# Optimization experiments

Measured on AMD Instinct MI355X. Metric: run time of the kernel, lower is better.

The kernel has to match this reference:

```python
import jax, jax.numpy as jnp
import numpy as np
import math

INPUT_SIZE = 1024
B, L1, L2 = 8, 2048, 2048


def setup_inputs() -> dict:
    key = jax.random.key(0)
    ks = jax.random.split(key, 10)
    s = 1.0 / math.sqrt(INPUT_SIZE)
    return {
        "Q": jax.random.normal(ks[0], (B, L1, INPUT_SIZE), dtype=jnp.float32),
        "K": jax.random.normal(ks[1], (B, L2, INPUT_SIZE), dtype=jnp.float32),
        "V": jax.random.normal(ks[2], (B, L2, INPUT_SIZE), dtype=jnp.float32),
        "K_mask": jax.random.randint(ks[3], (B, L2), 0, 2, dtype=jnp.int32),
        "Wq": jax.random.normal(ks[4], (INPUT_SIZE, INPUT_SIZE), dtype=jnp.float32) * s,
        "bq": jax.random.normal(ks[5], (INPUT_SIZE,), dtype=jnp.float32) * s,
        "Wk": jax.random.normal(ks[6], (INPUT_SIZE, INPUT_SIZE), dtype=jnp.float32) * s,
        "bk": jax.random.normal(ks[7], (INPUT_SIZE,), dtype=jnp.float32) * s,
        "Wv": jax.random.normal(ks[8], (INPUT_SIZE, INPUT_SIZE), dtype=jnp.float32) * s,
        "bv": jax.random.normal(ks[9], (INPUT_SIZE,), dtype=jnp.float32) * s,
    }


def reference(Q, K, V, K_mask, Wq, bq, Wk, bk, Wv, bv):
    # Linear projections (torch Linear: x @ W.T + b)
    q = jnp.einsum('bld,ed->ble', Q, Wq) + bq
    k = jnp.einsum('bld,ed->ble', K, Wk) + bk
    v = jnp.einsum('bld,ed->ble', V, Wv) + bv
    # scores: [B, L1, L2], scaled by sqrt(input_size)
    scores = jnp.einsum('bqd,bkd->bqk', q, k) / math.sqrt(INPUT_SIZE)
    # K_mask == 1 marks padding -> -inf before softmax
    scores = jnp.where(K_mask[:, None, :] == 1, -jnp.inf, scores)
    alpha = jax.nn.softmax(scores, axis=-1)
    matched_seq = jnp.einsum('bqk,bkd->bqd', alpha, v)
    return matched_seq
```

## Files before the change

kernel.cpp:

```cpp
#include <hip/hip_runtime.h>


using u16 = unsigned short;
using frag_ab = __attribute__((ext_vector_type(8))) short;
using frag_cd = __attribute__((ext_vector_type(4))) float;

#define BAR() asm volatile("s_barrier" ::: "memory")
#define WAITV(n) asm volatile("s_waitcnt vmcnt(" #n ")" ::: "memory")
#define L(d, ab, h) (lds + (((d) * 4) + ((ab) * 2) + (h)) * 8192)

__device__ __forceinline__ u16 f2bf(float f) {
  union { float f; unsigned u; } c; c.f = f;
  unsigned u = c.u;
  return (u16)((u + 0x7FFFu + ((u >> 16) & 1u)) >> 16);
}

__device__ __forceinline__ void async_ld16(const void* g, void* l) {
  __builtin_amdgcn_global_load_lds(
      (const __attribute__((address_space(1))) unsigned*)g,
      (__attribute__((address_space(3))) unsigned*)l, 16, 0, 0);
}

__global__ void cvt_f32_bf16(const float* __restrict__ in, u16* __restrict__ out, long n) {
  long i = ((long)blockIdx.x * 256 + threadIdx.x) * 4;
  if (i >= n) return;
  float4 v = *reinterpret_cast<const float4*>(in + i);
  ushort4 o = make_ushort4(f2bf(v.x), f2bf(v.y), f2bf(v.z), f2bf(v.w));
  *reinterpret_cast<ushort4*>(out + i) = o;
}

__device__ __forceinline__ void stage_half(const u16* __restrict__ g_rowbase,
                                           long Kstr, u16* l_half,
                                           int wave, int lane) {
  const int t = wave * 64 + lane;
  #pragma unroll
  for (int i = 0; i < 2; i++) {
    const int row = i * 64 + (t >> 3);
    const int cb  = (t & 7) * 16;
    const int cbs = cb ^ ((row & 7) << 4);
    async_ld16(g_rowbase + (long)row * Kstr + (cbs >> 1),
               l_half + i * 4096 + wave * 512);
  }
}

__device__ __forceinline__ frag_ab ld_frag(const u16* half_base, int r, int k) {
  const int idx = r * 64 + (k ^ ((r & 7) << 3));
  return *reinterpret_cast<const frag_ab*>(half_base + idx);
}

template<int OUT_MODE>
__device__ __forceinline__ void
gemm256_body(const u16* __restrict__ A, const u16* __restrict__ Bt,
             void* __restrict__ Cout, const float* __restrict__ bias,
             int M, int N, int K, long sA, long sB, long sC, float scale,
             u16* lds)
{
  const int gx = gridDim.x, gy = gridDim.y, gz = gridDim.z;
  const int nwg = gx * gy * gz;
  const int lin = ((int)blockIdx.z * gy + blockIdx.y) * gx + blockIdx.x;
  const int q8 = nwg >> 3, r8 = nwg & 7;
  const int xcd = lin & 7, idx8 = lin >> 3;
  const int swz = (xcd < r8 ? xcd * (q8 + 1) : r8 * (q8 + 1) + (xcd - r8) * q8) + idx8;
  const int z = swz / (gx * gy);
  const int rem = swz % (gx * gy);
  const int m0 = (rem / gx) * 256;
  const int n0 = (rem % gx) * 256;

  const u16* Ab = A + (long)z * sA;
  const u16* Bb = Bt + (long)z * sB;

  const int tid = threadIdx.x;
  const int wave = tid >> 6, lane = tid & 63;
  const int wm = wave >> 2;
  const int wn = wave & 3;
  const int ln15 = lane & 15, kof = (lane >> 4) * 8;
  const int rB0 = (wn & 1) * 64;
  const int NT = K >> 6;

  frag_cd acc[8][4];
  #pragma unroll
  for (int i = 0; i < 8; i++)
    #pragma unroll
    for (int j = 0; j < 4; j++)
      acc[i][j] = (frag_cd){0.f, 0.f, 0.f, 0.f};

  stage_half(Ab + (long)(m0 +   0) * K, K, L(0, 0, 0), wave, lane);
  stage_half(Ab + (long)(m0 + 128) * K, K, L(0, 0, 1), wave, lane);
  stage_half(Bb + (long)(n0 +   0) * K, K, L(0, 1, 0), wave, lane);
  stage_half(Bb + (long)(n0 + 128) * K, K, L(0, 1, 1), wave, lane);
  {
    const int t1 = (1 < NT) ? 1 : 0;
    stage_half(Bb + (long)(n0 +   0) * K + t1 * 64, K, L(1, 1, 0), wave, lane);
    stage_half(Bb + (long)(n0 + 128) * K + t1 * 64, K, L(1, 1, 1), wave, lane);
  }
  WAITV(4);
  BAR();

  for (int t = 0; t < NT; ++t) {
    const int d = t & 1;
    const u16* Al = L(d, 0, wm);
    const u16* Bl = L(d, 1, wn >> 1);
    const int tA = (t + 1 < NT) ? t + 1 : NT - 1;
    const int tB = (t + 2 < NT) ? t + 2 : NT - 1;

    frag_ab bf[4][2], af[2][2];

    #pragma unroll
    for (int bn = 0; bn < 4; ++bn)
      #pragma unroll
      for (int kk = 0; kk < 2; ++kk)
        bf[bn][kk] = ld_frag(Bl, rB0 + bn * 16 + ln15, kk * 32 + kof);
    #pragma unroll
    for (int am = 0; am < 2; ++am)
      #pragma unroll
      for (int kk = 0; kk < 2; ++kk)
        af[am][kk] = ld_frag(Al, am * 16 + ln15, kk * 32 + kof);
    stage_half(Ab + (long)(m0 +   0) * K + tA * 64, K, L(d ^ 1, 0, 0), wave, lane);
    stage_half(Ab + (long)(m0 + 128) * K + tA * 64, K, L(d ^ 1, 0, 1), wave, lane);
    BAR();
    __builtin_amdgcn_s_setprio(1);
    #pragma unroll
    for (int am = 0; am < 2; ++am)
      #pragma unroll
      for (int bn = 0; bn < 4; ++bn)
        #pragma unroll
        for (int kk = 0; kk < 2; ++kk)
          acc[am][bn] = __builtin_amdgcn_mfma_f32_16x16x32_bf16(af[am][kk], bf[bn][kk], acc[am][bn], 0, 0, 0);
    __builtin_amdgcn_s_setprio(0);
    BAR();

    #pragma unroll
    for (int am = 0; am < 2; ++am)
      #pragma unroll
      for (int kk = 0; kk < 2; ++kk)
        af[am][kk] = ld_frag(Al, (2 + am) * 16 + ln15, kk * 32 + kof);
    stage_half(Bb + (long)(n0 + 0) * K + tB * 64, K, L(d, 1, 0), wave, lane);
    BAR();
    __builtin_amdgcn_s_setprio(1);
    #pragma unroll
    for (int am = 0; am < 2; ++am)
      #pragma unroll
      for (int bn = 0; bn < 4; ++bn)
        #pragma unroll
        for (int kk = 0; kk < 2; ++kk)
          acc[2 + am][bn] = __builtin_amdgcn_mfma_f32_16x16x32_bf16(af[am][kk], bf[bn][kk], acc[2 + am][bn], 0, 0, 0);
    __builtin_amdgcn_s_setprio(0);
    BAR();

    #pragma unroll
    for (int am = 0; am < 2; ++am)
      #pragma unroll
      for (int kk = 0; kk < 2; ++kk)
        af[am][kk] = ld_frag(Al, (4 + am) * 16 + ln15, kk * 32 + kof);
    stage_half(Bb + (long)(n0 + 128) * K + tB * 64, K, L(d, 1, 1), wave, lane);
    BAR();
    __builtin_amdgcn_s_setprio(1);
    #pragma unroll
    for (int am = 0; am < 2; ++am)
      #pragma unroll
      for (int bn = 0; bn < 4; ++bn)
        #pragma unroll
        for (int kk = 0; kk < 2; ++kk)
          acc[4 + am][bn] = __builtin_amdgcn_mfma_f32_16x16x32_bf16(af[am][kk], bf[bn][kk], acc[4 + am][bn], 0, 0, 0);
    __builtin_amdgcn_s_setprio(0);
    BAR();

    #pragma unroll
    for (int am = 0; am < 2; ++am)
      #pragma unroll
      for (int kk = 0; kk < 2; ++kk)
        af[am][kk] = ld_frag(Al, (6 + am) * 16 + ln15, kk * 32 + kof);
    BAR();
    __builtin_amdgcn_s_setprio(1);
    #pragma unroll
    for (int am = 0; am < 2; ++am)
      #pragma unroll
      for (int bn = 0; bn < 4; ++bn)
        #pragma unroll
        for (int kk = 0; kk < 2; ++kk)
          acc[6 + am][bn] = __builtin_amdgcn_mfma_f32_16x16x32_bf16(af[am][kk], bf[bn][kk], acc[6 + am][bn], 0, 0, 0);
    __builtin_amdgcn_s_setprio(0);
    WAITV(4);
    BAR();
  }

  WAITV(0);
  BAR();

  const int cl = lane & 15;
  const int rb = (lane >> 4) * 4;
  #pragma unroll
  for (int bn = 0; bn < 4; ++bn) {
    const int gcol = n0 + wn * 64 + bn * 16 + cl;
    const float badd = bias ? bias[gcol] : 0.f;
    #pragma unroll
    for (int am = 0; am < 8; ++am) {
      #pragma unroll
      for (int r = 0; r < 4; ++r) {
        const int grow = m0 + wm * 128 + am * 16 + rb + r;
        const float val = acc[am][bn][r] * scale + badd;
        if (OUT_MODE == 0) {
          ((float*)Cout)[(long)z * sC + (long)grow * N + gcol] = val;
        } else if (OUT_MODE == 1) {
          ((u16*)Cout)[(long)z * sC + (long)grow * N + gcol] = f2bf(val);
        } else {
          const int bb = grow >> 11, l2 = grow & 2047;
          ((u16*)Cout)[((long)bb * N + gcol) * 2048 + l2] = f2bf(val);
        }
      }
    }
  }
}

__global__ void __launch_bounds__(512, 2)
proj_gemm(const u16* A, const u16* Bt, void* C, const float* bias,
          int M, int N, int K, long sA, long sB, long sC, float scale) {
  __shared__ u16 lds[8 * 8192];
  gemm256_body<1>(A, Bt, C, bias, M, N, K, sA, sB, sC, scale, lds);
}
__global__ void __launch_bounds__(512, 2)
projv_gemm(const u16* A, const u16* Bt, void* C, const float* bias,
           int M, int N, int K, long sA, long sB, long sC, float scale) {
  __shared__ u16 lds[8 * 8192];
  gemm256_body<2>(A, Bt, C, bias, M, N, K, sA, sB, sC, scale, lds);
}
__global__ void __launch_bounds__(512, 2)
qk_gemm(const u16* A, const u16* Bt, void* C, const float* bias,
        int M, int N, int K, long sA, long sB, long sC, float scale) {
  __shared__ u16 lds[8 * 8192];
  gemm256_body<0>(A, Bt, C, bias, M, N, K, sA, sB, sC, scale, lds);
}
__global__ void __launch_bounds__(512, 2)
pv_gemm(const u16* A, const u16* Bt, void* C, const float* bias,
        int M, int N, int K, long sA, long sB, long sC, float scale) {
  __shared__ u16 lds[8 * 8192];
  gemm256_body<0>(A, Bt, C, bias, M, N, K, sA, sB, sC, scale, lds);
}

__global__ void softmax_rows(const float* __restrict__ S, const int* __restrict__ Km,
                             u16* __restrict__ P)
{
  const long row = blockIdx.x;
  const int b = (int)(row >> 11);
  const float* s = S + row * 2048;
  const int* mask = Km + (long)b * 2048;
  u16* p = P + row * 2048;

  const int t = threadIdx.x;
  const int base = t * 8;

  float4 v0 = *reinterpret_cast<const float4*>(s + base);
  float4 v1 = *reinterpret_cast<const float4*>(s + base + 4);
  int4 mA = *reinterpret_cast<const int4*>(mask + base);
  int4 mB = *reinterpret_cast<const int4*>(mask + base + 4);

  float vals[8] = {v0.x, v0.y, v0.z, v0.w, v1.x, v1.y, v1.z, v1.w};
  const int mk[8] = {mA.x, mA.y, mA.z, mA.w, mB.x, mB.y, mB.z, mB.w};

  float mx = -3.0e38f;
  #pragma unroll
  for (int i = 0; i < 8; i++) if (!mk[i]) mx = fmaxf(mx, vals[i]);
  #pragma unroll
  for (int off = 32; off > 0; off >>= 1) mx = fmaxf(mx, __shfl_xor(mx, off));

  __shared__ float redm[4], reds[4];
  const int wave = t >> 6, lane = t & 63;
  if (lane == 0) redm[wave] = mx;
  __syncthreads();
  mx = fmaxf(fmaxf(redm[0], redm[1]), fmaxf(redm[2], redm[3]));

  float e[8]; float sum = 0.f;
  #pragma unroll
  for (int i = 0; i < 8; i++) { e[i] = mk[i] ? 0.f : __expf(vals[i] - mx); sum += e[i]; }
  #pragma unroll
  for (int off = 32; off > 0; off >>= 1) sum += __shfl_xor(sum, off);
  if (lane == 0) reds[wave] = sum;
  __syncthreads();
  sum = reds[0] + reds[1] + reds[2] + reds[3];
  const float inv = 1.f / sum;

  ushort4 o0 = make_ushort4(f2bf(e[0]*inv), f2bf(e[1]*inv), f2bf(e[2]*inv), f2bf(e[3]*inv));
  ushort4 o1 = make_ushort4(f2bf(e[4]*inv), f2bf(e[5]*inv), f2bf(e[6]*inv), f2bf(e[7]*inv));
  *reinterpret_cast<ushort4*>(p + base) = o0;
  *reinterpret_cast<ushort4*>(p + base + 4) = o1;
}

extern "C" void kernel_launch(void* const* d_in, const int* in_sizes, int n_in,
                              void* d_out, int out_size, void* d_ws, size_t ws_size,
                              hipStream_t stream) {
  (void)in_sizes; (void)n_in; (void)out_size;

  const float* Qin  = (const float*)d_in[0];
  const float* Kin  = (const float*)d_in[1];
  const float* Vin  = (const float*)d_in[2];
  const int*   Kmask = (const int*)d_in[3];
  const float* Wq = (const float*)d_in[4];
  const float* bq = (const float*)d_in[5];
  const float* Wk = (const float*)d_in[6];
  const float* bk = (const float*)d_in[7];
  const float* Wv = (const float*)d_in[8];
  const float* bv = (const float*)d_in[9];

  char* ws = (char*)d_ws;
  const size_t MB = 1024UL * 1024UL;
  const long NQKV = 8L * 2048 * 1024;
  const long NW = 1024L * 1024;
  const dim3 blk(256);
  const dim3 gblk(512);
  const float rs = 0.03125f;

  if (ws_size >= 226 * MB) {
    u16*  qb = (u16*)(ws);
    u16*  kb = (u16*)(ws + 32 * MB);
    u16*  vT = (u16*)(ws + 64 * MB);
    u16*  P  = (u16*)(ws + 96 * MB);
    u16*  Xb = (u16*)(ws + 96 * MB);
    float* S = (float*)(ws + 160 * MB);
    u16*  Wb = (u16*)(ws + 224 * MB);

    cvt_f32_bf16<<<dim3(NQKV / 1024), blk, 0, stream>>>(Qin, Xb, NQKV);
    cvt_f32_bf16<<<dim3(NW / 1024), blk, 0, stream>>>(Wq, Wb, NW);
    proj_gemm<<<dim3(4, 64, 1), gblk, 0, stream>>>(Xb, Wb, qb, bq,
        16384, 1024, 1024, 0, 0, 0, 1.f);

    cvt_f32_bf16<<<dim3(NQKV / 1024), blk, 0, stream>>>(Kin, Xb, NQKV);
    cvt_f32_bf16<<<dim3(NW / 1024), blk, 0, stream>>>(Wk, Wb, NW);
    proj_gemm<<<dim3(4, 64, 1), gblk, 0, stream>>>(Xb, Wb, kb, bk,
        16384, 1024, 1024, 0, 0, 0, 1.f);

    cvt_f32_bf16<<<dim3(NQKV / 1024), blk, 0, stream>>>(Vin, Xb, NQKV);
    cvt_f32_bf16<<<dim3(NW / 1024), blk, 0, stream>>>(Wv, Wb, NW);
    projv_gemm<<<dim3(4, 64, 1), gblk, 0, stream>>>(Xb, Wb, vT, bv,
        16384, 1024, 1024, 0, 0, 0, 1.f);

    for (int h = 0; h < 2; h++) {
      const u16* qbH = qb + (long)(4 * h) * 2048 * 1024;
      const u16* kbH = kb + (long)(4 * h) * 2048 * 1024;
      qk_gemm<<<dim3(8, 8, 4), gblk, 0, stream>>>(qbH, kbH, S, nullptr,
          2048, 2048, 1024, 2048L * 1024, 2048L * 1024, 2048L * 2048, rs);
      softmax_rows<<<dim3(8192), blk, 0, stream>>>(
          S, Kmask + (long)(4 * h) * 2048, P + (long)(4 * h) * 2048 * 2048);
    }

    pv_gemm<<<dim3(4, 8, 8), gblk, 0, stream>>>(P, vT, d_out, nullptr,
        2048, 1024, 2048, 2048L * 2048, 1024L * 2048, 2048L * 1024, 1.f);
  } else if (ws_size >= 194 * MB) {
    u16*  qb = (u16*)(ws);
    u16*  kb = (u16*)(ws + 32 * MB);
    u16*  vT = (u16*)(ws + 64 * MB);
    u16*  P  = (u16*)(ws + 96 * MB);
    u16*  Xb = (u16*)(ws + 96 * MB);
    float* S = (float*)(ws + 160 * MB);
    u16*  Wb = (u16*)(ws + 192 * MB);

    cvt_f32_bf16<<<dim3(NQKV / 1024), blk, 0, stream>>>(Qin, Xb, NQKV);
    cvt_f32_bf16<<<dim3(NW / 1024), blk, 0, stream>>>(Wq, Wb, NW);
    proj_gemm<<<dim3(4, 64, 1), gblk, 0, stream>>>(Xb, Wb, qb, bq,
        16384, 1024, 1024, 0, 0, 0, 1.f);

    cvt_f32_bf16<<<dim3(NQKV / 1024), blk, 0, stream>>>(Kin, Xb, NQKV);
    cvt_f32_bf16<<<dim3(NW / 1024), blk, 0, stream>>>(Wk, Wb, NW);
    proj_gemm<<<dim3(4, 64, 1), gblk, 0, stream>>>(Xb, Wb, kb, bk,
        16384, 1024, 1024, 0, 0, 0, 1.f);

    cvt_f32_bf16<<<dim3(NQKV / 1024), blk, 0, stream>>>(Vin, Xb, NQKV);
    cvt_f32_bf16<<<dim3(NW / 1024), blk, 0, stream>>>(Wv, Wb, NW);
    projv_gemm<<<dim3(4, 64, 1), gblk, 0, stream>>>(Xb, Wb, vT, bv,
        16384, 1024, 1024, 0, 0, 0, 1.f);

    for (int p = 0; p < 4; p++) {
      const u16* qbP = qb + (long)(2 * p) * 2048 * 1024;
      const u16* kbP = kb + (long)(2 * p) * 2048 * 1024;
      qk_gemm<<<dim3(8, 8, 2), gblk, 0, stream>>>(qbP, kbP, S, nullptr,
          2048, 2048, 1024, 2048L * 1024, 2048L * 1024, 2048L * 2048, rs);
      softmax_rows<<<dim3(4096), blk, 0, stream>>>(
          S, Kmask + (long)(2 * p) * 2048, P + (long)(2 * p) * 2048 * 2048);
    }

    pv_gemm<<<dim3(4, 8, 8), gblk, 0, stream>>>(P, vT, d_out, nullptr,
        2048, 1024, 2048, 2048L * 2048, 1024L * 2048, 2048L * 1024, 1.f);
  } else {
    u16*  qb = (u16*)(ws);
    u16*  kb = (u16*)(ws + 32 * MB);
    u16*  vT = (u16*)(ws + 64 * MB);
    u16*  Xb = (u16*)(ws + 96 * MB);
    float* S = (float*)(ws + 96 * MB);
    u16*  P  = (u16*)(ws + 112 * MB);
    u16*  Wb = (u16*)(ws + 128 * MB);

    cvt_f32_bf16<<<dim3(NQKV / 1024), blk, 0, stream>>>(Qin, Xb, NQKV);
    cvt_f32_bf16<<<dim3(NW / 1024), blk, 0, stream>>>(Wq, Wb, NW);
    proj_gemm<<<dim3(4, 64, 1), gblk, 0, stream>>>(Xb, Wb, qb, bq,
        16384, 1024, 1024, 0, 0, 0, 1.f);

    cvt_f32_bf16<<<dim3(NQKV / 1024), blk, 0, stream>>>(Kin, Xb, NQKV);
    cvt_f32_bf16<<<dim3(NW / 1024), blk, 0, stream>>>(Wk, Wb, NW);
    proj_gemm<<<dim3(4, 64, 1), gblk, 0, stream>>>(Xb, Wb, kb, bk,
        16384, 1024, 1024, 0, 0, 0, 1.f);

    cvt_f32_bf16<<<dim3(NQKV / 1024), blk, 0, stream>>>(Vin, Xb, NQKV);
    cvt_f32_bf16<<<dim3(NW / 1024), blk, 0, stream>>>(Wv, Wb, NW);
    projv_gemm<<<dim3(4, 64, 1), gblk, 0, stream>>>(Xb, Wb, vT, bv,
        16384, 1024, 1024, 0, 0, 0, 1.f);

    for (int b = 0; b < 8; b++) {
      const u16* qbB = qb + (long)b * 2048 * 1024;
      const u16* kbB = kb + (long)b * 2048 * 1024;
      const u16* vTB = vT + (long)b * 1024 * 2048;
      float* outB = (float*)d_out + (long)b * 2048 * 1024;

      qk_gemm<<<dim3(8, 8, 1), gblk, 0, stream>>>(qbB, kbB, S, nullptr,
          2048, 2048, 1024, 0, 0, 0, rs);
      softmax_rows<<<dim3(2048), blk, 0, stream>>>(S, Kmask + (long)b * 2048, P);
      pv_gemm<<<dim3(4, 8, 1), gblk, 0, stream>>>(P, vTB, outB, nullptr,
          2048, 1024, 2048, 0, 0, 0, 1.f);
    }
  }
}
```

Measured before the change: 383.1 us.

## Fuse fp32-to-bf16 activation conversion into projection GEMM A-tile loads

The projection GEMMs now read fp32 Q/K/V directly. Each thread loads float4 pairs into registers, packs them to bf16 and writes them into the swizzled LDS tile, interleaved with the MFMA phases. This removes three separate conversion kernels and their round trips through the 32MB bf16 staging buffer. In exchange the projection kernels drop to one workgroup per CU through launch bounds, use more registers, and lose the async direct-to-LDS path for A.

Result: slower. 405.1 us (+5.8%).

```diff
diff --git a/kernel.cpp b/kernel.cpp
--- a/kernel.cpp
+++ b/kernel.cpp
@@ -7,12 +7,23 @@
 
 #define BAR() asm volatile("s_barrier" ::: "memory")
 #define WAITV(n) asm volatile("s_waitcnt vmcnt(" #n ")" ::: "memory")
+#define WAITLGKM0() do { asm volatile("s_waitcnt lgkmcnt(0)" ::: "memory"); \
+                         __builtin_amdgcn_sched_barrier(0); } while (0)
 #define L(d, ab, h) (lds + (((d) * 4) + ((ab) * 2) + (h)) * 8192)
 
 __device__ __forceinline__ u16 f2bf(float f) {
   union { float f; unsigned u; } c; c.f = f;
   unsigned u = c.u;
   return (u16)((u + 0x7FFFu + ((u >> 16) & 1u)) >> 16);
+}
+
+__device__ __forceinline__ frag_ab pack8(float4 x, float4 y) {
+  frag_ab p;
+  p[0] = (short)f2bf(x.x); p[1] = (short)f2bf(x.y);
+  p[2] = (short)f2bf(x.z); p[3] = (short)f2bf(x.w);
+  p[4] = (short)f2bf(y.x); p[5] = (short)f2bf(y.y);
+  p[6] = (short)f2bf(y.z); p[7] = (short)f2bf(y.w);
+  return p;
 }
 
 __device__ __forceinline__ void async_ld16(const void* g, void* l) {
@@ -48,9 +59,13 @@
   return *reinterpret_cast<const frag_ab*>(half_base + idx);
 }
 
-template<int OUT_MODE>
+__device__ __forceinline__ void st_frag(u16* half_base, int r, int s, frag_ab v) {
+  *reinterpret_cast<frag_ab*>(half_base + r * 64 + ((s ^ (r & 7)) << 3)) = v;
+}
+
+template<int OUT_MODE, bool AF32>
 __device__ __forceinline__ void
-gemm256_body(const u16* __restrict__ A, const u16* __restrict__ Bt,
+gemm256_body(const void* __restrict__ Avoid, const u16* __restrict__ Bt,
              void* __restrict__ Cout, const float* __restrict__ bias,
              int M, int N, int K, long sA, long sB, long sC, float scale,
              u16* lds)
@@ -66,7 +81,8 @@
   const int m0 = (rem / gx) * 256;
   const int n0 = (rem % gx) * 256;
 
-  const u16* Ab = A + (long)z * sA;
+  const u16*   Ab16 = AF32 ? nullptr : (const u16*)Avoid + (long)z * sA;
+  const float* Abf  = AF32 ? (const float*)Avoid + (long)z * sA : nullptr;
   const u16* Bb = Bt + (long)z * sB;
 
   const int tid = threadIdx.x;
@@ -76,6 +92,8 @@
   const int ln15 = lane & 15, kof = (lane >> 4) * 8;
   const int rB0 = (wn & 1) * 64;
   const int NT = K >> 6;
+  const int sr = tid >> 3;
+  const int ss = tid & 7;
 
   frag_cd acc[8][4];
   #pragma unroll
@@ -84,17 +102,43 @@
     for (int j = 0; j < 4; j++)
       acc[i][j] = (frag_cd){0.f, 0.f, 0.f, 0.f};
 
-  stage_half(Ab + (long)(m0 +   0) * K, K, L(0, 0, 0), wave, lane);
-  stage_half(Ab + (long)(m0 + 128) * K, K, L(0, 0, 1), wave, lane);
-  stage_half(Bb + (long)(n0 +   0) * K, K, L(0, 1, 0), wave, lane);
-  stage_half(Bb + (long)(n0 + 128) * K, K, L(0, 1, 1), wave, lane);
-  {
-    const int t1 = (1 < NT) ? 1 : 0;
-    stage_half(Bb + (long)(n0 +   0) * K + t1 * 64, K, L(1, 1, 0), wave, lane);
-    stage_half(Bb + (long)(n0 + 128) * K + t1 * 64, K, L(1, 1, 1), wave, lane);
+  if (AF32) {
+    const float* a0 = Abf + (long)(m0 + sr) * K + ss * 8;
+    float4 c0a = *(const float4*)(a0);
+    float4 c0b = *(const float4*)(a0 + 4);
+    float4 c1a = *(const float4*)(a0 +  64L * K);
+    float4 c1b = *(const float4*)(a0 +  64L * K + 4);
+    float4 c2a = *(const float4*)(a0 + 128L * K);
+    float4 c2b = *(const float4*)(a0 + 128L * K + 4);
+    float4 c3a = *(const float4*)(a0 + 192L * K);
+    float4 c3b = *(const float4*)(a0 + 192L * K + 4);
+    stage_half(Bb + (long)(n0 +   0) * K, K, L(0, 1, 0), wave, lane);
+    stage_half(Bb + (long)(n0 + 128) * K, K, L(0, 1, 1), wave, lane);
+    {
+      const int t1 = (1 < NT) ? 1 : 0;
+      stage_half(Bb + (long)(n0 +   0) * K + t1 * 64, K, L(1, 1, 0), wave, lane);
+      stage_half(Bb + (long)(n0 + 128) * K + t1 * 64, K, L(1, 1, 1), wave, lane);
+    }
+    st_frag(L(0, 0, 0), sr,      ss, pack8(c0a, c0b));
+    st_frag(L(0, 0, 0), sr + 64, ss, pack8(c1a, c1b));
+    st_frag(L(0, 0, 1), sr,      ss, pack8(c2a, c2b));
+    st_frag(L(0, 0, 1), sr + 64, ss, pack8(c3a, c3b));
+    WAITV(0);
+    WAITLGKM0();
+    BAR();
+  } else {
+    stage_half(Ab16 + (long)(m0 +   0) * K, K, L(0, 0, 0), wave, lane);
+    stage_half(Ab16 + (long)(m0 + 128) * K, K, L(0, 0, 1), wave, lane);
+    stage_half(Bb + (long)(n0 +   0) * K, K, L(0, 1, 0), wave, lane);
+    stage_half(Bb + (long)(n0 + 128) * K, K, L(0, 1, 1), wave, lane);
+    {
+      const int t1 = (1 < NT) ? 1 : 0;
+      stage_half(Bb + (long)(n0 +   0) * K + t1 * 64, K, L(1, 1, 0), wave, lane);
+      stage_half(Bb + (long)(n0 + 128) * K + t1 * 64, K, L(1, 1, 1), wave, lane);
+    }
+    WAITV(4);
+    BAR();
   }
-  WAITV(4);
-  BAR();
 
   for (int t = 0; t < NT; ++t) {
     const int d = t & 1;
@@ -104,6 +148,7 @@
     const int tB = (t + 2 < NT) ? t + 2 : NT - 1;
 
     frag_ab bf[4][2], af[2][2];
+    float4 c0a, c0b, c1a, c1b, c2a, c2b, c3a, c3b;
 
     #pragma unroll
     for (int bn = 0; bn < 4; ++bn)
@@ -115,8 +160,16 @@
       #pragma unroll
       for (int kk = 0; kk < 2; ++kk)
         af[am][kk] = ld_frag(Al, am * 16 + ln15, kk * 32 + kof);
-    stage_half(Ab + (long)(m0 +   0) * K + tA * 64, K, L(d ^ 1, 0, 0), wave, lane);
-    stage_half(Ab + (long)(m0 + 128) * K + tA * 64, K, L(d ^ 1, 0, 1), wave, lane);
+    if (AF32) {
+      const float* ap = Abf + (long)(m0 + sr) * K + tA * 64 + ss * 8;
+      c0a = *(const float4*)(ap);
+      c0b = *(const float4*)(ap + 4);
+      c1a = *(const float4*)(ap + 64L * K);
+      c1b = *(const float4*)(ap + 64L * K + 4);
+    } else {
+      stage_half(Ab16 + (long)(m0 +   0) * K + tA * 64, K, L(d ^ 1, 0, 0), wave, lane);
+      stage_half(Ab16 + (long)(m0 + 128) * K + tA * 64, K, L(d ^ 1, 0, 1), wave, lane);
+    }
     BAR();
     __builtin_amdgcn_s_setprio(1);
     #pragma unroll
@@ -134,7 +187,18 @@
       #pragma unroll
       for (int kk = 0; kk < 2; ++kk)
         af[am][kk] = ld_frag(Al, (2 + am) * 16 + ln15, kk * 32 + kof);
+    if (AF32) {
+      const float* ap = Abf + (long)(m0 + 128 + sr) * K + tA * 64 + ss * 8;
+      c2a = *(const float4*)(ap);
+      c2b = *(const float4*)(ap + 4);
+      c3a = *(const float4*)(ap + 64L * K);
+      c3b = *(const float4*)(ap + 64L * K + 4);
+    }
     stage_half(Bb + (long)(n0 + 0) * K + tB * 64, K, L(d, 1, 0), wave, lane);
+    if (AF32) {
+      st_frag(L(d ^ 1, 0, 0), sr,      ss, pack8(c0a, c0b));
+      st_frag(L(d ^ 1, 0, 0), sr + 64, ss, pack8(c1a, c1b));
+    }
     BAR();
     __builtin_amdgcn_s_setprio(1);
     #pragma unroll
@@ -153,6 +217,11 @@
       for (int kk = 0; kk < 2; ++kk)
         af[am][kk] = ld_frag(Al, (4 + am) * 16 + ln15, kk * 32 + kof);
     stage_half(Bb + (long)(n0 + 128) * K + tB * 64, K, L(d, 1, 1), wave, lane);
+    if (AF32) {
+      st_frag(L(d ^ 1, 0, 1), sr,      ss, pack8(c2a, c2b));
+      st_frag(L(d ^ 1, 0, 1), sr + 64, ss, pack8(c3a, c3b));
+      WAITLGKM0();
+    }
     BAR();
     __builtin_amdgcn_s_setprio(1);
     #pragma unroll
@@ -180,7 +249,7 @@
         for (int kk = 0; kk < 2; ++kk)
           acc[6 + am][bn] = __builtin_amdgcn_mfma_f32_16x16x32_bf16(af[am][kk], bf[bn][kk], acc[6 + am][bn], 0, 0, 0);
     __builtin_amdgcn_s_setprio(0);
-    WAITV(4);
+    if (!AF32) { WAITV(4); }
     BAR();
   }
 
@@ -212,29 +281,29 @@
   }
 }
 
-__global__ void __launch_bounds__(512, 2)
-proj_gemm(const u16* A, const u16* Bt, void* C, const float* bias,
+__global__ void __launch_bounds__(512, 1)
+proj_gemm(const void* A, const u16* Bt, void* C, const float* bias,
           int M, int N, int K, long sA, long sB, long sC, float scale) {
   __shared__ u16 lds[8 * 8192];
-  gemm256_body<1>(A, Bt, C, bias, M, N, K, sA, sB, sC, scale, lds);
-}
-__global__ void __launch_bounds__(512, 2)
-projv_gemm(const u16* A, const u16* Bt, void* C, const float* bias,
+  gemm256_body<1, true>(A, Bt, C, bias, M, N, K, sA, sB, sC, scale, lds);
+}
+__global__ void __launch_bounds__(512, 1)
+projv_gemm(const void* A, const u16* Bt, void* C, const float* bias,
            int M, int N, int K, long sA, long sB, long sC, float scale) {
   __shared__ u16 lds[8 * 8192];
-  gemm256_body<2>(A, Bt, C, bias, M, N, K, sA, sB, sC, scale, lds);
+  gemm256_body<2, true>(A, Bt, C, bias, M, N, K, sA, sB, sC, scale, lds);
 }
 __global__ void __launch_bounds__(512, 2)
-qk_gemm(const u16* A, const u16* Bt, void* C, const float* bias,
+qk_gemm(const void* A, const u16* Bt, void* C, const float* bias,
         int M, int N, int K, long sA, long sB, long sC, float scale) {
   __shared__ u16 lds[8 * 8192];
-  gemm256_body<0>(A, Bt, C, bias, M, N, K, sA, sB, sC, scale, lds);
+  gemm256_body<0, false>(A, Bt, C, bias, M, N, K, sA, sB, sC, scale, lds);
 }
 __global__ void __launch_bounds__(512, 2)
-pv_gemm(const u16* A, const u16* Bt, void* C, const float* bias,
+pv_gemm(const void* A, const u16* Bt, void* C, const float* bias,
         int M, int N, int K, long sA, long sB, long sC, float scale) {
   __shared__ u16 lds[8 * 8192];
-  gemm256_body<0>(A, Bt, C, bias, M, N, K, sA, sB, sC, scale, lds);
+  gemm256_body<0, false>(A, Bt, C, bias, M, N, K, sA, sB, sC, scale, lds);
 }
 
 __global__ void softmax_rows(const float* __restrict__ S, const int* __restrict__ Km,
@@ -303,7 +372,6 @@
 
   char* ws = (char*)d_ws;
   const size_t MB = 1024UL * 1024UL;
-  const long NQKV = 8L * 2048 * 1024;
   const long NW = 1024L * 1024;
   const dim3 blk(256);
   const dim3 gblk(512);
@@ -314,23 +382,19 @@
     u16*  kb = (u16*)(ws + 32 * MB);
     u16*  vT = (u16*)(ws + 64 * MB);
     u16*  P  = (u16*)(ws + 96 * MB);
-    u16*  Xb = (u16*)(ws + 96 * MB);
     float* S = (float*)(ws + 160 * MB);
     u16*  Wb = (u16*)(ws + 224 * MB);
 
-    cvt_f32_bf16<<<dim3(NQKV / 1024), blk, 0, stream>>>(Qin, Xb, NQKV);
     cvt_f32_bf16<<<dim3(NW / 1024), blk, 0, stream>>>(Wq, Wb, NW);
-    proj_gemm<<<dim3(4, 64, 1), gblk, 0, stream>>>(Xb, Wb, qb, bq,
-        16384, 1024, 1024, 0, 0, 0, 1.f);
-
-    cvt_f32_bf16<<<dim3(NQKV / 1024), blk, 0, stream>>>(Kin, Xb, NQKV);
+    proj_gemm<<<dim3(4, 64, 1), gblk, 0, stream>>>(Qin, Wb, qb, bq,
+        16384, 1024, 1024, 0, 0, 0, 1.f);
+
     cvt_f32_bf16<<<dim3(NW / 1024), blk, 0, stream>>>(Wk, Wb, NW);
-    proj_gemm<<<dim3(4, 64, 1), gblk, 0, stream>>>(Xb, Wb, kb, bk,
-        16384, 1024, 1024, 0, 0, 0, 1.f);
-
-    cvt_f32_bf16<<<dim3(NQKV / 1024), blk, 0, stream>>>(Vin, Xb, NQKV);
+    proj_gemm<<<dim3(4, 64, 1), gblk, 0, stream>>>(Kin, Wb, kb, bk,
+        16384, 1024, 1024, 0, 0, 0, 1.f);
+
     cvt_f32_bf16<<<dim3(NW / 1024), blk, 0, stream>>>(Wv, Wb, NW);
-    projv_gemm<<<dim3(4, 64, 1), gblk, 0, stream>>>(Xb, Wb, vT, bv,
+    projv_gemm<<<dim3(4, 64, 1), gblk, 0, stream>>>(Vin, Wb, vT, bv,
         16384, 1024, 1024, 0, 0, 0, 1.f);
 
     for (int h = 0; h < 2; h++) {
@@ -349,23 +413,17 @@
     u16*  kb = (u16*)(ws + 32 * MB);
     u16*  vT = (u16*)(ws + 64 * MB);
     u16*  P  = (u16*)(ws + 96 * MB);
-    u16*  Xb = (u16*)(ws + 96 * MB);
     float* S = (float*)(ws + 160 * MB);
     u16*  Wb = (u16*)(ws + 192 * MB);
 
-    cvt_f32_bf16<<<dim3(NQKV / 1024), blk, 0, stream>>>(Qin, Xb, NQKV);
     cvt_f32_bf16<<<dim3(NW / 1024), blk, 0, stream>>>(Wq, Wb, NW);
-    proj_gemm<<<dim3(4, 64, 1), gblk, 0, stream>>>(Xb, Wb, qb, bq,
-        16384, 1024, 1024, 0, 0, 0, 1.f);
-
-    cvt_f32_bf16<<<dim3(NQKV / 1024), blk, 0, stream>>>(Kin, Xb, NQKV);
+    proj_gemm<<<dim3(4, 64, 1), gblk, 0, stream>>>(Qin, Wb, qb, bq,
+        16384, 1024, 1024, 0, 0, 0, 1.f);
     cvt_f32_bf16<<<dim3(NW / 1024), blk, 0, stream>>>(Wk, Wb, NW);
-    proj_gemm<<<dim3(4, 64, 1), gblk, 0, stream>>>(Xb, Wb, kb, bk,
-        16384, 1024, 1024, 0, 0, 0, 1.f);
-
-    cvt_f32_bf16<<<dim3(NQKV / 1024), blk, 0, stream>>>(Vin, Xb, NQKV);
+    proj_gemm<<<dim3(4, 64, 1), gblk, 0, stream>>>(Kin, Wb, kb, bk,
+        16384, 1024, 1024, 0, 0, 0, 1.f);
     cvt_f32_bf16<<<dim3(NW / 1024), blk, 0, stream>>>(Wv, Wb, NW);
-    projv_gemm<<<dim3(4, 64, 1), gblk, 0, stream>>>(Xb, Wb, vT, bv,
+    projv_gemm<<<dim3(4, 64, 1), gblk, 0, stream>>>(Vin, Wb, vT, bv,
         16384, 1024, 1024, 0, 0, 0, 1.f);
 
     for (int p = 0; p < 4; p++) {
@@ -383,24 +441,18 @@
     u16*  qb = (u16*)(ws);
     u16*  kb = (u16*)(ws + 32 * MB);
     u16*  vT = (u16*)(ws + 64 * MB);
-    u16*  Xb = (u16*)(ws + 96 * MB);
-    float* S = (float*)(ws + 96 * MB);
-    u16*  P  = (u16*)(ws + 112 * MB);
-    u16*  Wb = (u16*)(ws + 128 * MB);
-
-    cvt_f32_bf16<<<dim3(NQKV / 1024), blk, 0, stream>>>(Qin, Xb, NQKV);
+    float* S = (float*)(ws + 96 * MB + 2 * MB);
+    u16*  P  = (u16*)(ws + 96 * MB + 18 * MB);
+    u16*  Wb = (u16*)(ws + 96 * MB);
+
     cvt_f32_bf16<<<dim3(NW / 1024), blk, 0, stream>>>(Wq, Wb, NW);
-    proj_gemm<<<dim3(4, 64, 1), gblk, 0, stream>>>(Xb, Wb, qb, bq,
-        16384, 1024, 1024, 0, 0, 0, 1.f);
-
-    cvt_f32_bf16<<<dim3(NQKV / 1024), blk, 0, stream>>>(Kin, Xb, NQKV);
+    proj_gemm<<<dim3(4, 64, 1), gblk, 0, stream>>>(Qin, Wb, qb, bq,
+        16384, 1024, 1024, 0, 0, 0, 1.f);
     cvt_f32_bf16<<<dim3(NW / 1024), blk, 0, stream>>>(Wk, Wb, NW);
-    proj_gemm<<<dim3(4, 64, 1), gblk, 0, stream>>>(Xb, Wb, kb, bk,
-        16384, 1024, 1024, 0, 0, 0, 1.f);
-
-    cvt_f32_bf16<<<dim3(NQKV / 1024), blk, 0, stream>>>(Vin, Xb, NQKV);
+    proj_gemm<<<dim3(4, 64, 1), gblk, 0, stream>>>(Kin, Wb, kb, bk,
+        16384, 1024, 1024, 0, 0, 0, 1.f);
     cvt_f32_bf16<<<dim3(NW / 1024), blk, 0, stream>>>(Wv, Wb, NW);
-    projv_gemm<<<dim3(4, 64, 1), gblk, 0, stream>>>(Xb, Wb, vT, bv,
+    projv_gemm<<<dim3(4, 64, 1), gblk, 0, stream>>>(Vin, Wb, vT, bv,
         16384, 1024, 1024, 0, 0, 0, 1.f);
 
     for (int b = 0; b < 8; b++) {
```

## Store attention scores in fp16 and batch input conversion and QK launches

Applied to the files above, without the earlier changes.

The QK GEMM now writes scores as fp16 instead of fp32, and the softmax reads fp16. This halves the bytes of the largest intermediate written and then read back. The three fp32-to-bf16 input conversions are merged into one launch writing separate buffers. With the larger workspace, all 8 batches of the QK GEMM and softmax run in one launch each instead of a loop. The costs are some precision loss in the scores and extra workspace overlap that depends on launch ordering.

New measurement: 365.3 us. 1.05x faster.

```diff
diff --git a/kernel.cpp b/kernel.cpp
--- a/kernel.cpp
+++ b/kernel.cpp
@@ -14,6 +14,12 @@
   unsigned u = c.u;
   return (u16)((u + 0x7FFFu + ((u >> 16) & 1u)) >> 16);
 }
+__device__ __forceinline__ u16 f2h(float f) {
+  union { _Float16 h; u16 u; } c; c.h = (_Float16)f; return c.u;
+}
+__device__ __forceinline__ float h2f(u16 u) {
+  union { u16 u; _Float16 h; } c; c.u = u; return (float)c.h;
+}
 
 __device__ __forceinline__ void async_ld16(const void* g, void* l) {
   __builtin_amdgcn_global_load_lds(
@@ -25,8 +31,18 @@
   long i = ((long)blockIdx.x * 256 + threadIdx.x) * 4;
   if (i >= n) return;
   float4 v = *reinterpret_cast<const float4*>(in + i);
-  ushort4 o = make_ushort4(f2bf(v.x), f2bf(v.y), f2bf(v.z), f2bf(v.w));
-  *reinterpret_cast<ushort4*>(out + i) = o;
+  *reinterpret_cast<ushort4*>(out + i) =
+      make_ushort4(f2bf(v.x), f2bf(v.y), f2bf(v.z), f2bf(v.w));
+}
+
+__global__ void cvt3_f32_bf16(const float* __restrict__ q, const float* __restrict__ k,
+                              const float* __restrict__ v, u16* __restrict__ out) {
+  const float* in = blockIdx.z == 0 ? q : (blockIdx.z == 1 ? k : v);
+  u16* o = out + (long)blockIdx.z * 16777216L;
+  long i = ((long)blockIdx.x * 256 + threadIdx.x) * 4;
+  float4 x = *reinterpret_cast<const float4*>(in + i);
+  *reinterpret_cast<ushort4*>(o + i) =
+      make_ushort4(f2bf(x.x), f2bf(x.y), f2bf(x.z), f2bf(x.w));
 }
 
 __device__ __forceinline__ void stage_half(const u16* __restrict__ g_rowbase,
@@ -203,6 +219,8 @@
           ((float*)Cout)[(long)z * sC + (long)grow * N + gcol] = val;
         } else if (OUT_MODE == 1) {
           ((u16*)Cout)[(long)z * sC + (long)grow * N + gcol] = f2bf(val);
+        } else if (OUT_MODE == 3) {
+          ((u16*)Cout)[(long)z * sC + (long)grow * N + gcol] = f2h(val);
         } else {
           const int bb = grow >> 11, l2 = grow & 2047;
           ((u16*)Cout)[((long)bb * N + gcol) * 2048 + l2] = f2bf(val);
@@ -228,7 +246,7 @@
 qk_gemm(const u16* A, const u16* Bt, void* C, const float* bias,
         int M, int N, int K, long sA, long sB, long sC, float scale) {
   __shared__ u16 lds[8 * 8192];
-  gemm256_body<0>(A, Bt, C, bias, M, N, K, sA, sB, sC, scale, lds);
+  gemm256_body<3>(A, Bt, C, bias, M, N, K, sA, sB, sC, scale, lds);
 }
 __global__ void __launch_bounds__(512, 2)
 pv_gemm(const u16* A, const u16* Bt, void* C, const float* bias,
@@ -237,24 +255,25 @@
   gemm256_body<0>(A, Bt, C, bias, M, N, K, sA, sB, sC, scale, lds);
 }
 
-__global__ void softmax_rows(const float* __restrict__ S, const int* __restrict__ Km,
-                             u16* __restrict__ P)
+__global__ void softmax_rows_h(const u16* __restrict__ S, const int* __restrict__ Km,
+                               u16* __restrict__ P)
 {
   const long row = blockIdx.x;
   const int b = (int)(row >> 11);
-  const float* s = S + row * 2048;
+  const u16* s = S + row * 2048;
   const int* mask = Km + (long)b * 2048;
   u16* p = P + row * 2048;
 
   const int t = threadIdx.x;
   const int base = t * 8;
 
-  float4 v0 = *reinterpret_cast<const float4*>(s + base);
-  float4 v1 = *reinterpret_cast<const float4*>(s + base + 4);
+  ushort4 r0 = *reinterpret_cast<const ushort4*>(s + base);
+  ushort4 r1 = *reinterpret_cast<const ushort4*>(s + base + 4);
   int4 mA = *reinterpret_cast<const int4*>(mask + base);
   int4 mB = *reinterpret_cast<const int4*>(mask + base + 4);
 
-  float vals[8] = {v0.x, v0.y, v0.z, v0.w, v1.x, v1.y, v1.z, v1.w};
+  float vals[8] = {h2f(r0.x), h2f(r0.y), h2f(r0.z), h2f(r0.w),
+                   h2f(r1.x), h2f(r1.y), h2f(r1.z), h2f(r1.w)};
   const int mk[8] = {mA.x, mA.y, mA.z, mA.w, mB.x, mB.y, mB.z, mB.w};
 
   float mx = -3.0e38f;
@@ -279,10 +298,10 @@
   sum = reds[0] + reds[1] + reds[2] + reds[3];
   const float inv = 1.f / sum;
 
-  ushort4 o0 = make_ushort4(f2bf(e[0]*inv), f2bf(e[1]*inv), f2bf(e[2]*inv), f2bf(e[3]*inv));
-  ushort4 o1 = make_ushort4(f2bf(e[4]*inv), f2bf(e[5]*inv), f2bf(e[6]*inv), f2bf(e[7]*inv));
-  *reinterpret_cast<ushort4*>(p + base) = o0;
-  *reinterpret_cast<ushort4*>(p + base + 4) = o1;
+  *reinterpret_cast<ushort4*>(p + base) =
+      make_ushort4(f2bf(e[0]*inv), f2bf(e[1]*inv), f2bf(e[2]*inv), f2bf(e[3]*inv));
+  *reinterpret_cast<ushort4*>(p + base + 4) =
+      make_ushort4(f2bf(e[4]*inv), f2bf(e[5]*inv), f2bf(e[6]*inv), f2bf(e[7]*inv));
 }
 
 extern "C" void kernel_launch(void* const* d_in, const int* in_sizes, int n_in,
@@ -303,7 +322,6 @@
 
   char* ws = (char*)d_ws;
   const size_t MB = 1024UL * 1024UL;
-  const long NQKV = 8L * 2048 * 1024;
   const long NW = 1024L * 1024;
   const dim3 blk(256);
   const dim3 gblk(512);
@@ -314,33 +332,27 @@
     u16*  kb = (u16*)(ws + 32 * MB);
     u16*  vT = (u16*)(ws + 64 * MB);
     u16*  P  = (u16*)(ws + 96 * MB);
-    u16*  Xb = (u16*)(ws + 96 * MB);
-    float* S = (float*)(ws + 160 * MB);
+    u16*  Xq = (u16*)(ws + 96 * MB);
+    u16*  S  = (u16*)(ws + 160 * MB);
     u16*  Wb = (u16*)(ws + 224 * MB);
 
-    cvt_f32_bf16<<<dim3(NQKV / 1024), blk, 0, stream>>>(Qin, Xb, NQKV);
+    cvt3_f32_bf16<<<dim3(16384, 1, 3), blk, 0, stream>>>(Qin, Kin, Vin, Xq);
+
     cvt_f32_bf16<<<dim3(NW / 1024), blk, 0, stream>>>(Wq, Wb, NW);
-    proj_gemm<<<dim3(4, 64, 1), gblk, 0, stream>>>(Xb, Wb, qb, bq,
-        16384, 1024, 1024, 0, 0, 0, 1.f);
-
-    cvt_f32_bf16<<<dim3(NQKV / 1024), blk, 0, stream>>>(Kin, Xb, NQKV);
+    proj_gemm<<<dim3(4, 64, 1), gblk, 0, stream>>>(Xq, Wb, qb, bq,
+        16384, 1024, 1024, 0, 0, 0, 1.f);
+
     cvt_f32_bf16<<<dim3(NW / 1024), blk, 0, stream>>>(Wk, Wb, NW);
-    proj_gemm<<<dim3(4, 64, 1), gblk, 0, stream>>>(Xb, Wb, kb, bk,
-        16384, 1024, 1024, 0, 0, 0, 1.f);
-
-    cvt_f32_bf16<<<dim3(NQKV / 1024), blk, 0, stream>>>(Vin, Xb, NQKV);
+    proj_gemm<<<dim3(4, 64, 1), gblk, 0, stream>>>(Xq + 16777216L, Wb, kb, bk,
+        16384, 1024, 1024, 0, 0, 0, 1.f);
+
     cvt_f32_bf16<<<dim3(NW / 1024), blk, 0, stream>>>(Wv, Wb, NW);
-    projv_gemm<<<dim3(4, 64, 1), gblk, 0, stream>>>(Xb, Wb, vT, bv,
-        16384, 1024, 1024, 0, 0, 0, 1.f);
-
-    for (int h = 0; h < 2; h++) {
-      const u16* qbH = qb + (long)(4 * h) * 2048 * 1024;
-      const u16* kbH = kb + (long)(4 * h) * 2048 * 1024;
-      qk_gemm<<<dim3(8, 8, 4), gblk, 0, stream>>>(qbH, kbH, S, nullptr,
-          2048, 2048, 1024, 2048L * 1024, 2048L * 1024, 2048L * 2048, rs);
-      softmax_rows<<<dim3(8192), blk, 0, stream>>>(
-          S, Kmask + (long)(4 * h) * 2048, P + (long)(4 * h) * 2048 * 2048);
-    }
+    projv_gemm<<<dim3(4, 64, 1), gblk, 0, stream>>>(Xq + 2L * 16777216L, Wb, vT, bv,
+        16384, 1024, 1024, 0, 0, 0, 1.f);
+
+    qk_gemm<<<dim3(8, 8, 8), gblk, 0, stream>>>(qb, kb, S, nullptr,
+        2048, 2048, 1024, 2048L * 1024, 2048L * 1024, 2048L * 2048, rs);
+    softmax_rows_h<<<dim3(16384), blk, 0, stream>>>(S, Kmask, P);
 
     pv_gemm<<<dim3(4, 8, 8), gblk, 0, stream>>>(P, vT, d_out, nullptr,
         2048, 1024, 2048, 2048L * 2048, 1024L * 2048, 2048L * 1024, 1.f);
@@ -349,32 +361,29 @@
     u16*  kb = (u16*)(ws + 32 * MB);
     u16*  vT = (u16*)(ws + 64 * MB);
     u16*  P  = (u16*)(ws + 96 * MB);
-    u16*  Xb = (u16*)(ws + 96 * MB);
-    float* S = (float*)(ws + 160 * MB);
+    u16*  Xq = (u16*)(ws + 96 * MB);
+    u16*  S  = (u16*)(ws + 160 * MB);
     u16*  Wb = (u16*)(ws + 192 * MB);
 
-    cvt_f32_bf16<<<dim3(NQKV / 1024), blk, 0, stream>>>(Qin, Xb, NQKV);
+    cvt3_f32_bf16<<<dim3(16384, 1, 3), blk, 0, stream>>>(Qin, Kin, Vin, Xq);
+
     cvt_f32_bf16<<<dim3(NW / 1024), blk, 0, stream>>>(Wq, Wb, NW);
-    proj_gemm<<<dim3(4, 64, 1), gblk, 0, stream>>>(Xb, Wb, qb, bq,
-        16384, 1024, 1024, 0, 0, 0, 1.f);
-
-    cvt_f32_bf16<<<dim3(NQKV / 1024), blk, 0, stream>>>(Kin, Xb, NQKV);
+    proj_gemm<<<dim3(4, 64, 1), gblk, 0, stream>>>(Xq, Wb, qb, bq,
+        16384, 1024, 1024, 0, 0, 0, 1.f);
     cvt_f32_bf16<<<dim3(NW / 1024), blk, 0, stream>>>(Wk, Wb, NW);
-    proj_gemm<<<dim3(4, 64, 1), gblk, 0, stream>>>(Xb, Wb, kb, bk,
-        16384, 1024, 1024, 0, 0, 0, 1.f);
-
-    cvt_f32_bf16<<<dim3(NQKV / 1024), blk, 0, stream>>>(Vin, Xb, NQKV);
+    proj_gemm<<<dim3(4, 64, 1), gblk, 0, stream>>>(Xq + 16777216L, Wb, kb, bk,
+        16384, 1024, 1024, 0, 0, 0, 1.f);
     cvt_f32_bf16<<<dim3(NW / 1024), blk, 0, stream>>>(Wv, Wb, NW);
-    projv_gemm<<<dim3(4, 64, 1), gblk, 0, stream>>>(Xb, Wb, vT, bv,
-        16384, 1024, 1024, 0, 0, 0, 1.f);
-
-    for (int p = 0; p < 4; p++) {
-      const u16* qbP = qb + (long)(2 * p) * 2048 * 1024;
-      const u16* kbP = kb + (long)(2 * p) * 2048 * 1024;
-      qk_gemm<<<dim3(8, 8, 2), gblk, 0, stream>>>(qbP, kbP, S, nullptr,
+    projv_gemm<<<dim3(4, 64, 1), gblk, 0, stream>>>(Xq + 2L * 16777216L, Wb, vT, bv,
+        16384, 1024, 1024, 0, 0, 0, 1.f);
+
+    for (int h = 0; h < 2; h++) {
+      const u16* qbH = qb + (long)(4 * h) * 2048 * 1024;
+      const u16* kbH = kb + (long)(4 * h) * 2048 * 1024;
+      qk_gemm<<<dim3(8, 8, 4), gblk, 0, stream>>>(qbH, kbH, S, nullptr,
           2048, 2048, 1024, 2048L * 1024, 2048L * 1024, 2048L * 2048, rs);
-      softmax_rows<<<dim3(4096), blk, 0, stream>>>(
-          S, Kmask + (long)(2 * p) * 2048, P + (long)(2 * p) * 2048 * 2048);
+      softmax_rows_h<<<dim3(8192), blk, 0, stream>>>(
+          S, Kmask + (long)(4 * h) * 2048, P + (long)(4 * h) * 2048 * 2048);
     }
 
     pv_gemm<<<dim3(4, 8, 8), gblk, 0, stream>>>(P, vT, d_out, nullptr,
@@ -384,20 +393,19 @@
     u16*  kb = (u16*)(ws + 32 * MB);
     u16*  vT = (u16*)(ws + 64 * MB);
     u16*  Xb = (u16*)(ws + 96 * MB);
-    float* S = (float*)(ws + 96 * MB);
-    u16*  P  = (u16*)(ws + 112 * MB);
+    u16*  S  = (u16*)(ws + 96 * MB);
+    u16*  P  = (u16*)(ws + 104 * MB);
     u16*  Wb = (u16*)(ws + 128 * MB);
+    const long NQKV = 8L * 2048 * 1024;
 
     cvt_f32_bf16<<<dim3(NQKV / 1024), blk, 0, stream>>>(Qin, Xb, NQKV);
     cvt_f32_bf16<<<dim3(NW / 1024), blk, 0, stream>>>(Wq, Wb, NW);
     proj_gemm<<<dim3(4, 64, 1), gblk, 0, stream>>>(Xb, Wb, qb, bq,
         16384, 1024, 1024, 0, 0, 0, 1.f);
-
     cvt_f32_bf16<<<dim3(NQKV / 1024), blk, 0, stream>>>(Kin, Xb, NQKV);
     cvt_f32_bf16<<<dim3(NW / 1024), blk, 0, stream>>>(Wk, Wb, NW);
     proj_gemm<<<dim3(4, 64, 1), gblk, 0, stream>>>(Xb, Wb, kb, bk,
         16384, 1024, 1024, 0, 0, 0, 1.f);
-
     cvt_f32_bf16<<<dim3(NQKV / 1024), blk, 0, stream>>>(Vin, Xb, NQKV);
     cvt_f32_bf16<<<dim3(NW / 1024), blk, 0, stream>>>(Wv, Wb, NW);
     projv_gemm<<<dim3(4, 64, 1), gblk, 0, stream>>>(Xb, Wb, vT, bv,
@@ -411,7 +419,7 @@
 
       qk_gemm<<<dim3(8, 8, 1), gblk, 0, stream>>>(qbB, kbB, S, nullptr,
           2048, 2048, 1024, 0, 0, 0, rs);
-      softmax_rows<<<dim3(2048), blk, 0, stream>>>(S, Kmask + (long)b * 2048, P);
+      softmax_rows_h<<<dim3(2048), blk, 0, stream>>>(S, Kmask + (long)b * 2048, P);
       pv_gemm<<<dim3(4, 8, 1), gblk, 0, stream>>>(P, vTB, outB, nullptr,
           2048, 1024, 2048, 0, 0, 0, 1.f);
     }
```
